# Kernel tuning notes

Hardware: AMD Instinct MI355X
Metric: run time of the kernel (lower is better)

## Reference

```python
import jax, jax.numpy as jnp
from jax import lax
import numpy as np

N_T = 70            # linspace(0, 60, 70) RK4 grid
STATE_DIM = 12
NOISE_STD = 0.01
T0 = jnp.linspace(0.0, 60.0, N_T)
DEFAULT_TIMES = jnp.array([0, 2, 4, 6, 8, 10, 12, 14, 16, 18, 20, 25, 30, 40, 50, 60], dtype=jnp.float32)
EPORA_DATA = jnp.array([0.01713, 0.145, 0.2442, 0.7659, 1.0, 0.8605, 0.7829, 0.5705,
                        0.6217, 0.331, 0.3388, 0.3116, 0.05062, 0.02504, 0.01163, 0.01163], dtype=jnp.float32)
PARAM_SHIFT = jnp.array([0.5, 0.05, 4.0], dtype=jnp.float32)
PARAM_SCALE = jnp.array([2.5, 0.15, 6.0], dtype=jnp.float32)


def _deriv(x, k1, k2, tau, E):
    # x: [B, 12]; k1,k2,tau: [B]; E: scalar EpoRA(t)
    x1, x2, x3 = x[:, 0], x[:, 1], x[:, 2]
    q1, q2, q3, q4, q5, q6, q7, out = (x[:, 4], x[:, 5], x[:, 6], x[:, 7],
                                       x[:, 8], x[:, 9], x[:, 10], x[:, 11])
    r = 8.0 / tau
    return jnp.stack([
        -k1 * x1 * E + k2 * out,
        -x2 * x2 + k1 * x1 * E,
        -k2 * x3 + x2 * x2,
        -k2 * out + k2 * x3,
        r * (x3 - q1),
        r * (q1 - q2),
        r * (q2 - q3),
        r * (q3 - q4),
        r * (q4 - q5),
        r * (q5 - q6),
        r * (q6 - q7),
        r * (q7 - out),
    ], axis=1)


def _simulate(ps):
    # ps: [B, 3] transformed parameters -> trajectory [N_T, B, 12]
    B = ps.shape[0]
    k1, k2, tau = ps[:, 0], ps[:, 1], ps[:, 2]
    dt = T0[1] - T0[0]
    t_start = T0[:-1]
    # EpoRA is a function of t only: precompute at the 3 RK4 stage times per step
    e_lo = jnp.interp(t_start, DEFAULT_TIMES, EPORA_DATA)
    e_mid = jnp.interp(t_start + 0.5 * dt, DEFAULT_TIMES, EPORA_DATA)
    e_hi = jnp.interp(t_start + dt, DEFAULT_TIMES, EPORA_DATA)
    x0 = jnp.zeros((B, STATE_DIM), dtype=ps.dtype).at[:, 0].set(3.71)

    def step(x, es):
        ea, eb, ec = es
        s1 = _deriv(x, k1, k2, tau, ea)
        s2 = _deriv(x + 0.5 * dt * s1, k1, k2, tau, eb)
        s3 = _deriv(x + 0.5 * dt * s2, k1, k2, tau, eb)
        s4 = _deriv(x + dt * s3, k1, k2, tau, ec)
        xn = x + (dt / 6.0) * (s1 + 2.0 * s2 + 2.0 * s3 + s4)
        return xn, xn

    _, traj = lax.scan(step, x0, (e_lo, e_mid, e_hi))
    return jnp.concatenate([x0[None], traj], axis=0)  # [70, B, 12]


def _forward(parameters, design):
    ps = PARAM_SHIFT + jax.scipy.stats.norm.cdf(parameters) * PARAM_SCALE  # [B,3]
    sol = _simulate(ps)                                   # [70, B, 12]
    y1 = 0.33 * (sol[:, :, 1] + sol[:, :, 2]).T           # [B, 70]
    y2 = 0.26 * (sol[:, :, 0] + sol[:, :, 1] + sol[:, :, 2]).T
    interp = jax.vmap(lambda yb: jnp.interp(design, T0, yb))
    return jnp.concatenate([interp(y1), interp(y2)], axis=1)  # [B, 2*obs_dim]


def setup_inputs() -> dict:
    key = jax.random.key(0)
    k1, k2, k3 = jax.random.split(key, 3)
    B, OBS = 65536, 8
    parameters = jax.random.normal(k1, (B, 3), dtype=jnp.float32)
    design = jnp.sort(60.0 * jax.random.uniform(k2, (OBS,), dtype=jnp.float32))
    noise = jax.random.normal(k3, (B, 2 * OBS), dtype=jnp.float32)
    return {"parameters": parameters, "design": design, "noise": noise}


def reference(parameters, design, noise):
    true_obs = _forward(parameters, design)
    noised_obs = true_obs + NOISE_STD * noise
    return true_obs, noised_obs
```

## Files before the change

kernel.cpp:

```cpp
#include <hip/hip_runtime.h>
#include <math.h>

#define NSTEP 69
#define OBS 8

namespace {

constexpr float kDT = 60.0f / 69.0f;

constexpr float interp_e(float t) {
    constexpr float DTm[16] = {0.f,2.f,4.f,6.f,8.f,10.f,12.f,14.f,16.f,18.f,20.f,25.f,30.f,40.f,50.f,60.f};
    constexpr float EP[16]  = {0.01713f,0.145f,0.2442f,0.7659f,1.0f,0.8605f,0.7829f,0.5705f,
                               0.6217f,0.331f,0.3388f,0.3116f,0.05062f,0.02504f,0.01163f,0.01163f};
    if (t >= 60.0f) return EP[15];
    if (t <= 0.0f)  return EP[0];
    int k = 0;
    for (int m = 0; m < 15; m++) if (t >= DTm[m]) k = m;
    float u = (t - DTm[k]) / (DTm[k + 1] - DTm[k]);
    return EP[k] + u * (EP[k + 1] - EP[k]);
}

struct EQuad { float lo, mid, hi, pad; };
struct ETab4 { EQuad q[NSTEP + 1]; };

constexpr ETab4 make_etab4() {
    ETab4 e{};
    for (int s = 0; s < NSTEP; s++) {
        float t0 = (float)s * kDT;
        e.q[s].lo  = interp_e(t0);
        e.q[s].mid = interp_e(t0 + 0.5f * kDT);
        e.q[s].hi  = interp_e(t0 + kDT);
        e.q[s].pad = 0.0f;
    }
    e.q[NSTEP] = e.q[NSTEP - 1];
    return e;
}

}

__constant__ ETab4 ETAB4 = make_etab4();

__global__ __launch_bounds__(256, 1) void stats5_kernel(
    const float* __restrict__ params,
    const float* __restrict__ design,
    const float* __restrict__ noise,
    float* __restrict__ out,
    int B)
{
    int b = blockIdx.x * blockDim.x + threadIdx.x;
    if (b >= B) return;

    int ij[OBS], ij1[OBS]; float wj[OBS], w1j[OBS];
    #pragma unroll
    for (int j = 0; j < OBS; j++) {
        float pos = design[j] * (1.0f / kDT);
        int i = (int)pos;
        i = i < 0 ? 0 : (i > NSTEP - 1 ? NSTEP - 1 : i);
        float w = pos - (float)i;
        ij[j]  = __builtin_amdgcn_readfirstlane(i);
        ij1[j] = ij[j] + 1;
        int wb = __builtin_amdgcn_readfirstlane(__float_as_int(w));
        wj[j]  = __int_as_float(wb);
        w1j[j] = 1.0f - wj[j];
    }

    unsigned long long m_lo = 0ull, m_hi = 0ull;
    #pragma unroll
    for (int j = 0; j < OBS; j++) {
        if (ij[j]  < 64) m_lo |= 1ull << ij[j];  else m_hi |= 1ull << (ij[j]  - 64);
        if (ij1[j] < 64) m_lo |= 1ull << ij1[j]; else m_hi |= 1ull << (ij1[j] - 64);
    }

    float p0 = params[3 * b], p1 = params[3 * b + 1], p2 = params[3 * b + 2];
    const float INV_SQRT2 = 0.7071067811865476f;
    float k1  = fmaf(0.5f * erfcf(-p0 * INV_SQRT2), 2.5f,  0.5f);
    float k2  = fmaf(0.5f * erfcf(-p1 * INV_SQRT2), 0.15f, 0.05f);
    float tau = fmaf(0.5f * erfcf(-p2 * INV_SQRT2), 6.0f,  4.0f);
    float r   = 8.0f / tau;

    const float hdt = 0.5f * kDT;
    const float c6  = kDT * (1.0f / 6.0f);
    const float k2r = 0.125f * k2 * tau;
    const float crh = hdt * r;
    const float crf = kDT * r;
    const float c6r = c6 * r;

    long long base = (long long)b * 16;
    long long nb   = (long long)B * 16;
    const float4* nz = (const float4*)(noise + base);
    float4 n0 = nz[0], n1 = nz[1], n2 = nz[2], n3 = nz[3];

    float a12[OBS], a0[OBS], b12[OBS], b0[OBS];
    #pragma unroll
    for (int j = 0; j < OBS; j++) { a12[j] = 0.f; a0[j] = 0.f; b12[j] = 0.f; b0[j] = 0.f; }

    float x0 = 3.71f, x1 = 0.f, x2 = 0.f;
    float W[8];
    #pragma unroll
    for (int i = 0; i < 8; i++) W[i] = 0.f;

    if (m_lo & 1ull) {
        #pragma unroll
        for (int j = 0; j < OBS; j++)
            if (ij[j] == 0) { a12[j] = 0.f; a0[j] = 3.71f; }
    }

    auto DERIV = [&](float k1E, float X0, float X1, float X2, const float* V,
                     float& D0, float& D1, float& D2, float* G) {
        float a  = k1E * X0;
        float sq = X1 * X1;
        D0 = fmaf(k2r, V[7], -a);
        D1 = a - sq;
        D2 = fmaf(-k2, X2, sq);
        G[0] = fmaf(r, X2, -V[0]);
        #pragma unroll
        for (int i = 1; i < 8; i++) G[i] = V[i - 1] - V[i];
    };

    const float4* et = reinterpret_cast<const float4*>(&ETAB4.q[0].lo);
    float4 eC = et[0];

    #pragma unroll 1
    for (int s = 0; s < NSTEP; s++) {
        float4 eN = et[s + 1];
        const float ea = eC.x, eb = eC.y, ec = eC.z;
        float k1a = k1 * ea, k1b = k1 * eb, k1c = k1 * ec;

        float d10, d11, d12, G1[8];
        DERIV(k1a, x0, x1, x2, W, d10, d11, d12, G1);

        float t0 = fmaf(hdt, d10, x0);
        float t1 = fmaf(hdt, d11, x1);
        float t2 = fmaf(hdt, d12, x2);
        float U[8];
        #pragma unroll
        for (int i = 0; i < 8; i++) U[i] = fmaf(crh, G1[i], W[i]);

        float d20, d21, d22, G2[8];
        DERIV(k1b, t0, t1, t2, U, d20, d21, d22, G2);

        float ax0 = fmaf(2.0f, d20, d10);
        float ax1 = fmaf(2.0f, d21, d11);
        float ax2 = fmaf(2.0f, d22, d12);
        float A[8];
        #pragma unroll
        for (int i = 0; i < 8; i++) A[i] = fmaf(2.0f, G2[i], G1[i]);

        t0 = fmaf(hdt, d20, x0);
        t1 = fmaf(hdt, d21, x1);
        t2 = fmaf(hdt, d22, x2);
        #pragma unroll
        for (int i = 0; i < 8; i++) U[i] = fmaf(crh, G2[i], W[i]);

        float d30, d31, d32, G3[8];
        DERIV(k1b, t0, t1, t2, U, d30, d31, d32, G3);

        ax0 = fmaf(2.0f, d30, ax0);
        ax1 = fmaf(2.0f, d31, ax1);
        ax2 = fmaf(2.0f, d32, ax2);
        #pragma unroll
        for (int i = 0; i < 8; i++) A[i] = fmaf(2.0f, G3[i], A[i]);

        t0 = fmaf(kDT, d30, x0);
        t1 = fmaf(kDT, d31, x1);
        t2 = fmaf(kDT, d32, x2);
        #pragma unroll
        for (int i = 0; i < 8; i++) U[i] = fmaf(crf, G3[i], W[i]);

        float d40, d41, d42, G4[8];
        DERIV(k1c, t0, t1, t2, U, d40, d41, d42, G4);

        ax0 += d40; ax1 += d41; ax2 += d42;
        x0 = fmaf(c6, ax0, x0);
        x1 = fmaf(c6, ax1, x1);
        x2 = fmaf(c6, ax2, x2);
        #pragma unroll
        for (int i = 0; i < 8; i++) {
            float Ai = A[i] + G4[i];
            W[i] = fmaf(c6r, Ai, W[i]);
        }

        const int ti = s + 1;
        unsigned long long mm = (ti < 64) ? (m_lo >> ti) : (m_hi >> (ti - 64));
        if (__builtin_expect((int)(mm & 1ull), 0)) {
            float s12 = x1 + x2;
            #pragma unroll
            for (int j = 0; j < OBS; j++) {
                if (ti == ij[j])  { a12[j] = s12; a0[j] = x0; }
                if (ti == ij1[j]) { b12[j] = s12; b0[j] = x0; }
            }
        }
        eC = eN;
    }

    float o1[OBS], o2[OBS];
    #pragma unroll
    for (int j = 0; j < OBS; j++) {
        o1[j] = 0.33f * fmaf(w1j[j], a12[j], wj[j] * b12[j]);
        o2[j] = 0.26f * fmaf(w1j[j], a0[j] + a12[j], wj[j] * (b0[j] + b12[j]));
    }

    float4* outv = (float4*)(out + base);
    float4* outn = (float4*)(out + nb + base);

    float4 v0 = make_float4(o1[0], o1[1], o1[2], o1[3]);
    float4 v1 = make_float4(o1[4], o1[5], o1[6], o1[7]);
    float4 v2 = make_float4(o2[0], o2[1], o2[2], o2[3]);
    float4 v3 = make_float4(o2[4], o2[5], o2[6], o2[7]);
    outv[0] = v0; outv[1] = v1; outv[2] = v2; outv[3] = v3;

    outn[0] = make_float4(fmaf(0.01f, n0.x, v0.x), fmaf(0.01f, n0.y, v0.y),
                          fmaf(0.01f, n0.z, v0.z), fmaf(0.01f, n0.w, v0.w));
    outn[1] = make_float4(fmaf(0.01f, n1.x, v1.x), fmaf(0.01f, n1.y, v1.y),
                          fmaf(0.01f, n1.z, v1.z), fmaf(0.01f, n1.w, v1.w));
    outn[2] = make_float4(fmaf(0.01f, n2.x, v2.x), fmaf(0.01f, n2.y, v2.y),
                          fmaf(0.01f, n2.z, v2.z), fmaf(0.01f, n2.w, v2.w));
    outn[3] = make_float4(fmaf(0.01f, n3.x, v3.x), fmaf(0.01f, n3.y, v3.y),
                          fmaf(0.01f, n3.z, v3.z), fmaf(0.01f, n3.w, v3.w));
}

extern "C" void kernel_launch(void* const* d_in, const int* in_sizes, int n_in,
                              void* d_out, int out_size, void* d_ws, size_t ws_size,
                              hipStream_t stream) {
    const float* params = (const float*)d_in[0];
    const float* design = (const float*)d_in[1];
    const float* noise  = (const float*)d_in[2];
    float* out = (float*)d_out;
    int B = in_sizes[0] / 3;
    int block = 256;
    int grid = (B + block - 1) / block;
    stats5_kernel<<<grid, block, 0, stream>>>(params, design, noise, out, B);
}
```

Measured before the change: 90.46 us.

## Split each batch element's RK4 delay chain across four lanes using DPP quad shuffles

Each batch element is now handled by a quad of four lanes, each owning two of the eight delay-chain states. Neighbouring and final chain values are exchanged with DPP quad_perm moves, and each lane loads and stores one float4 of noise and output. The grid is four times larger and launch bounds now allow four blocks per CU. The aim is more waves per SIMD to hide the latency of the serial RK4 dependency chain, at the cost of repeating the three-state nonlinear part in every lane plus extra cross-lane moves.

```diff
diff --git a/kernel.cpp b/kernel.cpp
--- a/kernel.cpp
+++ b/kernel.cpp
@@ -40,15 +40,26 @@
 
 __constant__ ETab4 ETAB4 = make_etab4();
 
-__global__ __launch_bounds__(256, 1) void stats5_kernel(
+template <int CTRL>
+__device__ __forceinline__ float qperm(float x) {
+    return __int_as_float(
+        __builtin_amdgcn_mov_dpp(__float_as_int(x), CTRL, 0xf, 0xf, true));
+}
+#define QP_SHIFT 0x90
+#define QP_BC3   0xFF
+
+__global__ __launch_bounds__(256, 4) void stats5_kernel(
     const float* __restrict__ params,
     const float* __restrict__ design,
     const float* __restrict__ noise,
     float* __restrict__ out,
     int B)
 {
-    int b = blockIdx.x * blockDim.x + threadIdx.x;
+    int tid = blockIdx.x * blockDim.x + threadIdx.x;
+    int b   = tid >> 2;
+    int p   = threadIdx.x & 3;
     if (b >= B) return;
+    const bool isL0 = (p == 0);
 
     int ij[OBS], ij1[OBS]; float wj[OBS], w1j[OBS];
     #pragma unroll
@@ -87,17 +98,14 @@
 
     long long base = (long long)b * 16;
     long long nb   = (long long)B * 16;
-    const float4* nz = (const float4*)(noise + base);
-    float4 n0 = nz[0], n1 = nz[1], n2 = nz[2], n3 = nz[3];
+    float4 nmy = ((const float4*)(noise + base))[p];
 
     float a12[OBS], a0[OBS], b12[OBS], b0[OBS];
     #pragma unroll
     for (int j = 0; j < OBS; j++) { a12[j] = 0.f; a0[j] = 0.f; b12[j] = 0.f; b0[j] = 0.f; }
 
     float x0 = 3.71f, x1 = 0.f, x2 = 0.f;
-    float W[8];
-    #pragma unroll
-    for (int i = 0; i < 8; i++) W[i] = 0.f;
+    float WL = 0.f, WH = 0.f;
 
     if (m_lo & 1ull) {
         #pragma unroll
@@ -105,16 +113,18 @@
             if (ij[j] == 0) { a12[j] = 0.f; a0[j] = 3.71f; }
     }
 
-    auto DERIV = [&](float k1E, float X0, float X1, float X2, const float* V,
-                     float& D0, float& D1, float& D2, float* G) {
+    auto DERIV = [&](float k1E, float X0, float X1, float X2, float VL, float VH,
+                     float& D0, float& D1, float& D2, float& GL, float& GH) {
+        float vprev = qperm<QP_SHIFT>(VH);
+        float wout  = qperm<QP_BC3>(VH);
+        float prev  = isL0 ? (r * X2) : vprev;
         float a  = k1E * X0;
         float sq = X1 * X1;
-        D0 = fmaf(k2r, V[7], -a);
+        D0 = fmaf(k2r, wout, -a);
         D1 = a - sq;
         D2 = fmaf(-k2, X2, sq);
-        G[0] = fmaf(r, X2, -V[0]);
-        #pragma unroll
-        for (int i = 1; i < 8; i++) G[i] = V[i - 1] - V[i];
+        GL = prev - VL;
+        GH = VL - VH;
     };
 
     const float4* et = reinterpret_cast<const float4*>(&ETAB4.q[0].lo);
@@ -126,59 +136,49 @@
         const float ea = eC.x, eb = eC.y, ec = eC.z;
         float k1a = k1 * ea, k1b = k1 * eb, k1c = k1 * ec;
 
-        float d10, d11, d12, G1[8];
-        DERIV(k1a, x0, x1, x2, W, d10, d11, d12, G1);
-
+        float d10, d11, d12, G1L, G1H;
+        DERIV(k1a, x0, x1, x2, WL, WH, d10, d11, d12, G1L, G1H);
         float t0 = fmaf(hdt, d10, x0);
         float t1 = fmaf(hdt, d11, x1);
         float t2 = fmaf(hdt, d12, x2);
-        float U[8];
-        #pragma unroll
-        for (int i = 0; i < 8; i++) U[i] = fmaf(crh, G1[i], W[i]);
-
-        float d20, d21, d22, G2[8];
-        DERIV(k1b, t0, t1, t2, U, d20, d21, d22, G2);
-
+        float UL = fmaf(crh, G1L, WL);
+        float UH = fmaf(crh, G1H, WH);
+
+        float d20, d21, d22, G2L, G2H;
+        DERIV(k1b, t0, t1, t2, UL, UH, d20, d21, d22, G2L, G2H);
         float ax0 = fmaf(2.0f, d20, d10);
         float ax1 = fmaf(2.0f, d21, d11);
         float ax2 = fmaf(2.0f, d22, d12);
-        float A[8];
-        #pragma unroll
-        for (int i = 0; i < 8; i++) A[i] = fmaf(2.0f, G2[i], G1[i]);
-
+        float AL  = fmaf(2.0f, G2L, G1L);
+        float AH  = fmaf(2.0f, G2H, G1H);
         t0 = fmaf(hdt, d20, x0);
         t1 = fmaf(hdt, d21, x1);
         t2 = fmaf(hdt, d22, x2);
-        #pragma unroll
-        for (int i = 0; i < 8; i++) U[i] = fmaf(crh, G2[i], W[i]);
-
-        float d30, d31, d32, G3[8];
-        DERIV(k1b, t0, t1, t2, U, d30, d31, d32, G3);
-
+        UL = fmaf(crh, G2L, WL);
+        UH = fmaf(crh, G2H, WH);
+
+        float d30, d31, d32, G3L, G3H;
+        DERIV(k1b, t0, t1, t2, UL, UH, d30, d31, d32, G3L, G3H);
         ax0 = fmaf(2.0f, d30, ax0);
         ax1 = fmaf(2.0f, d31, ax1);
         ax2 = fmaf(2.0f, d32, ax2);
-        #pragma unroll
-        for (int i = 0; i < 8; i++) A[i] = fmaf(2.0f, G3[i], A[i]);
-
+        AL  = fmaf(2.0f, G3L, AL);
+        AH  = fmaf(2.0f, G3H, AH);
         t0 = fmaf(kDT, d30, x0);
         t1 = fmaf(kDT, d31, x1);
         t2 = fmaf(kDT, d32, x2);
-        #pragma unroll
-        for (int i = 0; i < 8; i++) U[i] = fmaf(crf, G3[i], W[i]);
-
-        float d40, d41, d42, G4[8];
-        DERIV(k1c, t0, t1, t2, U, d40, d41, d42, G4);
-
+        UL = fmaf(crf, G3L, WL);
+        UH = fmaf(crf, G3H, WH);
+
+        float d40, d41, d42, G4L, G4H;
+        DERIV(k1c, t0, t1, t2, UL, UH, d40, d41, d42, G4L, G4H);
         ax0 += d40; ax1 += d41; ax2 += d42;
         x0 = fmaf(c6, ax0, x0);
         x1 = fmaf(c6, ax1, x1);
         x2 = fmaf(c6, ax2, x2);
-        #pragma unroll
-        for (int i = 0; i < 8; i++) {
-            float Ai = A[i] + G4[i];
-            W[i] = fmaf(c6r, Ai, W[i]);
-        }
+        AL += G4L; AH += G4H;
+        WL = fmaf(c6r, AL, WL);
+        WH = fmaf(c6r, AH, WH);
 
         const int ti = s + 1;
         unsigned long long mm = (ti < 64) ? (m_lo >> ti) : (m_hi >> (ti - 64));
@@ -200,23 +200,17 @@
         o2[j] = 0.26f * fmaf(w1j[j], a0[j] + a12[j], wj[j] * (b0[j] + b12[j]));
     }
 
-    float4* outv = (float4*)(out + base);
-    float4* outn = (float4*)(out + nb + base);
-
     float4 v0 = make_float4(o1[0], o1[1], o1[2], o1[3]);
     float4 v1 = make_float4(o1[4], o1[5], o1[6], o1[7]);
     float4 v2 = make_float4(o2[0], o2[1], o2[2], o2[3]);
     float4 v3 = make_float4(o2[4], o2[5], o2[6], o2[7]);
-    outv[0] = v0; outv[1] = v1; outv[2] = v2; outv[3] = v3;
-
-    outn[0] = make_float4(fmaf(0.01f, n0.x, v0.x), fmaf(0.01f, n0.y, v0.y),
-                          fmaf(0.01f, n0.z, v0.z), fmaf(0.01f, n0.w, v0.w));
-    outn[1] = make_float4(fmaf(0.01f, n1.x, v1.x), fmaf(0.01f, n1.y, v1.y),
-                          fmaf(0.01f, n1.z, v1.z), fmaf(0.01f, n1.w, v1.w));
-    outn[2] = make_float4(fmaf(0.01f, n2.x, v2.x), fmaf(0.01f, n2.y, v2.y),
-                          fmaf(0.01f, n2.z, v2.z), fmaf(0.01f, n2.w, v2.w));
-    outn[3] = make_float4(fmaf(0.01f, n3.x, v3.x), fmaf(0.01f, n3.y, v3.y),
-                          fmaf(0.01f, n3.z, v3.z), fmaf(0.01f, n3.w, v3.w));
+
+    float4 mine = (p == 0) ? v0 : (p == 1) ? v1 : (p == 2) ? v2 : v3;
+
+    ((float4*)(out + base))[p] = mine;
+    ((float4*)(out + nb + base))[p] =
+        make_float4(fmaf(0.01f, nmy.x, mine.x), fmaf(0.01f, nmy.y, mine.y),
+                    fmaf(0.01f, nmy.z, mine.z), fmaf(0.01f, nmy.w, mine.w));
 }
 
 extern "C" void kernel_launch(void* const* d_in, const int* in_sizes, int n_in,
@@ -228,6 +222,7 @@
     float* out = (float*)d_out;
     int B = in_sizes[0] / 3;
     int block = 256;
-    int grid = (B + block - 1) / block;
+    long long threads = (long long)B * 4;
+    int grid = (int)((threads + block - 1) / block);
     stats5_kernel<<<grid, block, 0, stream>>>(params, design, noise, out, B);
 }
```

Measured after the change: 102.1 us. 1.13x slower.
